# Optimization experiments

Measured on AMD Instinct MI355X. Metric: run time of the kernel, lower is better.

Reference implementation:

```python
import jax, jax.numpy as jnp
import numpy as np

N_HASHES = 4
CHUNK = 144
REDUCTION = 4

# PyTorch bicubic (a=-0.75), align_corners=False, integer scale 2 ->
# fixed fractional offsets t=0.75 (even outputs) and t=0.25 (odd outputs).
_EW = jnp.array([-0.03515625, 0.26171875, 0.87890625, -0.10546875], jnp.float32)
_OW = _EW[::-1]


def _up2_axis(x, axis):
    n = x.shape[axis]
    pad = [(0, 0)] * x.ndim
    pad[axis] = (2, 2)
    xp = jnp.pad(x, pad, mode='edge')  # torch clamps border indices
    sl = lambda s: jax.lax.slice_in_dim(xp, s, s + n, axis=axis)
    even = sum(_EW[k] * sl(k) for k in range(4))
    odd = sum(_OW[k] * sl(k + 1) for k in range(4))
    out = jnp.stack([even, odd], axis=axis + 1)
    shp = list(x.shape)
    shp[axis] = 2 * n
    return out.reshape(shp)


def bicubic_up2(x):
    return _up2_axis(_up2_axis(x, 2), 3)


def conv2d(x, w, b, pad):
    y = jax.lax.conv_general_dilated(x, w, (1, 1), [(pad, pad), (pad, pad)],
                                     dimension_numbers=('NCHW', 'OIHW', 'NCHW'))
    return y + b[None, :, None, None]


def _adj(t):
    # attend to own + two adjacent buckets along chunk axis (axis=2)
    return jnp.concatenate([t, jnp.roll(t, 1, axis=2), jnp.roll(t, -1, axis=2)], axis=3)


def nlsa(x, wm, bm, wa, ba, rot):
    N, Cc, H, W = x.shape
    L = H * W
    xe = conv2d(x, wm, bm, 1).reshape(N, -1, L).transpose(0, 2, 1)  # [N,L,C]
    ye = conv2d(x, wa, ba, 0).reshape(N, -1, L).transpose(0, 2, 1)  # [N,L,C*red]
    C = xe.shape[-1]
    hash_buckets = min(L // CHUNK + (L // CHUNK) % 2, 128)
    # LSH: random rotations -> argmax bucket codes (non-differentiable, detached)
    rotated = jnp.einsum('btf,fhi->bhti', xe, rot)  # [N,h,L,hb//2]
    rotated = jnp.concatenate([rotated, -rotated], axis=-1)  # [N,h,L,hb]
    codes = jnp.argmax(rotated, axis=-1)  # [N,h,L]
    codes = codes + (jnp.arange(N_HASHES) * hash_buckets)[None, :, None]
    codes = jax.lax.stop_gradient(codes.reshape(N, -1))  # [N,h*L]
    indices = jnp.argsort(codes, axis=-1)
    undo = jnp.argsort(indices, axis=-1)
    mod = indices % L
    xs = jnp.take_along_axis(xe, mod[..., None], axis=1)  # [N,h*L,C]
    ys = jnp.take_along_axis(ye, mod[..., None], axis=1)  # [N,h*L,C*red]
    padding = (-L) % CHUNK
    xb = xs.reshape(N, N_HASHES, L, C)
    yb = ys.reshape(N, N_HASHES, L, C * REDUCTION)
    if padding:
        xb = jnp.concatenate([xb, xb[:, :, -padding:, :]], axis=2)
        yb = jnp.concatenate([yb, yb[:, :, -padding:, :]], axis=2)
    nch = xb.shape[2] // CHUNK
    xb = xb.reshape(N, N_HASHES, nch, CHUNK, C)
    yb = yb.reshape(N, N_HASHES, nch, CHUNK, C * REDUCTION)
    xm = xb / jnp.maximum(jnp.linalg.norm(xb, axis=-1, keepdims=True), 5e-5)
    xm = _adj(xm)      # [N,h,k,3*chunk,C]
    ybj = _adj(yb)     # [N,h,k,3*chunk,C*red]
    raw = jnp.einsum('bhkie,bhkje->bhkij', xb, xm)  # [N,h,k,chunk,3*chunk]
    bscore = jax.scipy.special.logsumexp(raw, axis=-1, keepdims=True)
    score = jnp.exp(raw - bscore)
    ret = jnp.einsum('bhkij,bhkje->bhkie', score, ybj)
    ret = ret.reshape(N, N_HASHES, -1, C * REDUCTION)
    bscore = bscore.reshape(N, N_HASHES, -1)
    if padding:
        ret = ret[:, :, :-padding]
        bscore = bscore[:, :, :-padding]
    ret = ret.reshape(N, -1, C * REDUCTION)
    bscore = bscore.reshape(N, -1)
    ret = jnp.take_along_axis(ret, undo[..., None], axis=1)
    bscore = jnp.take_along_axis(bscore, undo, axis=1)
    ret = ret.reshape(N, N_HASHES, L, C * REDUCTION)
    probs = jax.nn.softmax(bscore.reshape(N, N_HASHES, L, 1), axis=1)
    ret = jnp.sum(ret * probs, axis=1)  # [N,L,C*red]
    return ret.transpose(0, 2, 1).reshape(N, -1, H, W) + x


def setup_inputs() -> dict:
    key = jax.random.key(0)
    ks = jax.random.split(key, 8)
    w = lambda k, shape, fan: (jax.random.normal(k, shape, jnp.float32) / np.sqrt(fan)).astype(jnp.float32)
    return {
        'x': jax.random.normal(ks[0], (2, 64, 96, 96), jnp.float32),
        'w1': w(ks[1], (64, 64, 3, 3), 64 * 9), 'b1': jnp.zeros((64,), jnp.float32),
        'w2': w(ks[2], (64, 64, 3, 3), 64 * 9), 'b2': jnp.zeros((64,), jnp.float32),
        'wm': w(ks[3], (16, 64, 3, 3), 64 * 9), 'bm': jnp.zeros((16,), jnp.float32),
        'wa': w(ks[4], (64, 64, 1, 1), 64), 'ba': jnp.zeros((64,), jnp.float32),
        'rot': jax.random.normal(ks[5], (16, N_HASHES, 64), jnp.float32),  # [C, h, hash_buckets//2]
    }


def reference(x, w1, b1, w2, b2, wm, bm, wa, ba, rot):
    x = bicubic_up2(x)
    x = jax.nn.relu(conv2d(x, w1, b1, 1))
    x = jax.nn.relu(conv2d(x, w2, b2, 1))
    return nlsa(x, wm, bm, wa, ba, rot)
```

## Files before the change

kernel.cpp:

```cpp
#include <hip/hip_runtime.h>
#include <math.h>

#define NB 2
#define CIN 64
#define H0 96
#define W0 96
#define HH 192
#define WW 192
#define LL (HH*WW)
#define NHASH 4
#define CHK 144
#define NCHK 256
#define CE 16
#define NBUCK 128
#define SEGL 576
#define NSEG 64
#define PW 194
#define PS ((size_t)NB*PW*PW*64)

#define K_ROWB   80
#define V_ROWB   912
#define P_ROWB   72
#define VT_SZB   58368
#define PST_SZB  10368
#define LKI_SZB  1728
#define LDS_T1   (VT_SZB + PST_SZB + LKI_SZB)
#define CONV_LDS (2*4*66*64*2)

typedef __attribute__((ext_vector_type(8))) short short8_t;
typedef __attribute__((ext_vector_type(4))) float f32x4;
union FragU { unsigned int u[4]; int4 i; short8_t s; };

__device__ __forceinline__ unsigned int cvtpk_bf16(float a, float b){
  unsigned int r;
  asm("v_cvt_pk_bf16_f32 %0, %1, %2" : "=v"(r) : "v"(a), "v"(b));
  return r;
}
__device__ __forceinline__ float bfl(unsigned int u){ return __uint_as_float(u << 16); }
__device__ __forceinline__ float bfh(unsigned int u){ return __uint_as_float(u & 0xffff0000u); }

__global__ __launch_bounds__(256) void k_zerob(unsigned short* pA, unsigned short* pB){
  const int cid = blockIdx.x*256 + threadIdx.x;
  if (cid >= 4*2*772*8) return;
  const int chunk = cid & 7;
  int cell = cid >> 3;
  const int plane = cell / (2*772); cell -= plane*(2*772);
  const int n = cell / 772; int b = cell - n*772;
  int ypad, xpad;
  if (b < 194){ ypad = 0; xpad = b; }
  else if (b < 388){ ypad = 193; xpad = b-194; }
  else if (b < 580){ ypad = b-388+1; xpad = 0; }
  else { ypad = b-580+1; xpad = 193; }
  unsigned short* base = (plane < 2 ? pA : pB) + (size_t)(plane & 1)*PS;
  *(uint4*)(base + (((size_t)n*PW + ypad)*PW + xpad)*64 + chunk*8) =
      make_uint4(0u,0u,0u,0u);
}

__global__ __launch_bounds__(256) void k_upsample2(const float* __restrict__ x,
    unsigned short* __restrict__ oh, unsigned short* __restrict__ ol){
  __shared__ unsigned int pk[64][65];
  const int t = threadIdx.x;
  const int bx = blockIdx.x, oy = blockIdx.y, n = blockIdx.z;
  const int oxl = t & 63, cq = t >> 6;
  const int ox = bx*64 + oxl;
  const int i = oy >> 1, a = oy & 1;
  const int j = ox >> 1, b = ox & 1;
  const float e0=-0.03515625f, e1=0.26171875f, e2=0.87890625f, e3=-0.10546875f;
  float wy[4], wx[4]; int ty[4], tx[4];
  if (a){ wy[0]=e3; wy[1]=e2; wy[2]=e1; wy[3]=e0; } else { wy[0]=e0; wy[1]=e1; wy[2]=e2; wy[3]=e3; }
  if (b){ wx[0]=e3; wx[1]=e2; wx[2]=e1; wx[3]=e0; } else { wx[0]=e0; wx[1]=e1; wx[2]=e2; wx[3]=e3; }
  const int offy = a ? -1 : -2, offx = b ? -1 : -2;
  #pragma unroll
  for (int k=0;k<4;k++){
    int u = i + offy + k; ty[k] = u<0?0:(u>H0-1?H0-1:u);
    int s = j + offx + k; tx[k] = s<0?0:(s>W0-1?W0-1:s);
  }
  for (int ci = cq*16; ci < cq*16+16; ++ci){
    const float* xp = x + ((size_t)n*CIN + ci)*(H0*W0);
    float s = 0.f;
    #pragma unroll
    for (int ky=0;ky<4;ky++){
      const float* row = xp + ty[ky]*W0;
      float rs = 0.f;
      rs = fmaf(wx[0], row[tx[0]], rs);
      rs = fmaf(wx[1], row[tx[1]], rs);
      rs = fmaf(wx[2], row[tx[2]], rs);
      rs = fmaf(wx[3], row[tx[3]], rs);
      s = fmaf(wy[ky], rs, s);
    }
    unsigned int hu = cvtpk_bf16(s, s);
    unsigned int lu = cvtpk_bf16(s - bfl(hu), 0.f);
    pk[oxl][ci] = (hu & 0xffffu) | (lu << 16);
  }
  __syncthreads();
  const size_t rowb = (((size_t)n*PW + oy+1)*PW + bx*64 + 1)*64;
  for (int e = t; e < 1024; e += 256){
    const int plane = e >> 9, r2 = e & 511;
    const int ox2 = r2 >> 3, c8 = r2 & 7;
    const int xpad = bx*64 + ox2 + 1;
    const int grp = (c8 ^ (xpad & 7))*8;
    unsigned int a0=pk[ox2][grp+0], a1=pk[ox2][grp+1], a2=pk[ox2][grp+2], a3=pk[ox2][grp+3];
    unsigned int a4=pk[ox2][grp+4], a5=pk[ox2][grp+5], a6=pk[ox2][grp+6], a7=pk[ox2][grp+7];
    uint4 wv;
    if (plane == 0){
      wv.x = (a0&0xffffu)|(a1<<16); wv.y = (a2&0xffffu)|(a3<<16);
      wv.z = (a4&0xffffu)|(a5<<16); wv.w = (a6&0xffffu)|(a7<<16);
    } else {
      wv.x = (a0>>16)|(a1&0xffff0000u); wv.y = (a2>>16)|(a3&0xffff0000u);
      wv.z = (a4>>16)|(a5&0xffff0000u); wv.w = (a6>>16)|(a7&0xffff0000u);
    }
    *(uint4*)((plane ? ol : oh) + rowb + (size_t)ox2*64 + c8*8) = wv;
  }
}

__global__ __launch_bounds__(256) void k_prepw(const float* __restrict__ w,
    unsigned short* __restrict__ wsT, int CO){
  int idx = blockIdx.x*256 + threadIdx.x;
  if (idx >= CO*64*9) return;
  int tap = idx % 9; int rem = idx / 9;
  int ci = rem % 64; int co = rem / 64;
  float v = w[(size_t)(co*64 + ci)*9 + tap];
  unsigned int hu = cvtpk_bf16(v, v) & 0xffffu;
  float hf = bfl(hu);
  unsigned int lu = cvtpk_bf16(v - hf, 0.f) & 0xffffu;
  int half = ci >> 5, kg = (ci >> 3) & 3, e = ci & 7;
  size_t base = ((size_t)(tap*2 + half)*2)*CO*32 + ((size_t)co*4 + kg)*8 + e;
  wsT[base]         = (unsigned short)hu;
  wsT[base + (size_t)CO*32] = (unsigned short)lu;
}

template<int CO, int OMODE>
__global__ __launch_bounds__(256) void k_conv3s(const unsigned short* __restrict__ inh,
    const unsigned short* __restrict__ inl, const unsigned short* __restrict__ wsT,
    const float* __restrict__ bias, unsigned short* __restrict__ outh,
    unsigned short* __restrict__ outl, float* __restrict__ outf){
  extern __shared__ char cvsm[];
  unsigned short (*inH)[66][64] = (unsigned short (*)[66][64])cvsm;
  unsigned short (*inL)[66][64] = (unsigned short (*)[66][64])(cvsm + 33792);
  const int t = threadIdx.x;
  const int bx = blockIdx.x, by = blockIdx.y, n = blockIdx.z;
  const int y0 = by*2, x0 = bx*64;
  const int l = t & 63, w = t >> 6;
  const int lq = l & 15, kg = l >> 4;

  const size_t gbase = (((size_t)n*PW + y0)*PW + x0)*64;
  for (int e = t; e < 4224; e += 256){
    const int plane = (e >= 2112);
    const int rem = e - plane*2112;
    const int row = rem / 528;
    const int cw = rem - row*528;
    const unsigned short* src = (plane ? inl : inh) + gbase + (size_t)row*(PW*64) + cw*8;
    *(uint4*)(cvsm + plane*33792 + row*8448 + cw*16) = *(const uint4*)src;
  }
  __syncthreads();

  constexpr int NCT = CO/16;
  f32x4 acc0[NCT], acc1[NCT];
  #pragma unroll
  for (int c=0;c<NCT;c++){ acc0[c] = (f32x4){0.f,0.f,0.f,0.f}; acc1[c] = acc0[c]; }
  const unsigned short* wlane = wsT + (size_t)lq*32 + (size_t)kg*8;

  #pragma unroll
  for (int tap=0; tap<9; ++tap){
    const int ky = tap/3, kx = tap - ky*3;
    const int col = w*16 + lq + kx;
    #pragma unroll
    for (int half=0; half<2; ++half){
      const int sci = ((((half<<2) | kg) ^ (col & 7)) << 3);
      FragU Bh0, Bl0, Bh1, Bl1;
      Bh0.i = *(const int4*)&inH[ky  ][col][sci];
      Bl0.i = *(const int4*)&inL[ky  ][col][sci];
      Bh1.i = *(const int4*)&inH[ky+1][col][sci];
      Bl1.i = *(const int4*)&inL[ky+1][col][sci];
      const unsigned short* wth = wlane + (size_t)((tap*2+half)*2)*CO*32;
      #pragma unroll
      for (int ct=0; ct<NCT; ++ct){
        FragU Ah, Al;
        Ah.i = *(const int4*)(wth + ct*512);
        Al.i = *(const int4*)(wth + CO*32 + ct*512);
        acc0[ct] = __builtin_amdgcn_mfma_f32_16x16x32_bf16(Ah.s, Bl0.s, acc0[ct], 0,0,0);
        acc0[ct] = __builtin_amdgcn_mfma_f32_16x16x32_bf16(Al.s, Bh0.s, acc0[ct], 0,0,0);
        acc0[ct] = __builtin_amdgcn_mfma_f32_16x16x32_bf16(Ah.s, Bh0.s, acc0[ct], 0,0,0);
        acc1[ct] = __builtin_amdgcn_mfma_f32_16x16x32_bf16(Ah.s, Bl1.s, acc1[ct], 0,0,0);
        acc1[ct] = __builtin_amdgcn_mfma_f32_16x16x32_bf16(Al.s, Bh1.s, acc1[ct], 0,0,0);
        acc1[ct] = __builtin_amdgcn_mfma_f32_16x16x32_bf16(Ah.s, Bh1.s, acc1[ct], 0,0,0);
      }
    }
  }

  const int px = x0 + w*16 + lq;
  const int xpad = px + 1;
  const int xg = xpad & 7;
  if constexpr (OMODE == 2){
    #pragma unroll
    for (int r=0; r<4; ++r){
      const int co = kg*4 + r;
      const float bv = bias[co];
      outf[((size_t)n*LL + (size_t)(y0  )*WW + px)*16 + co] = acc0[0][r] + bv;
      outf[((size_t)n*LL + (size_t)(y0+1)*WW + px)*16 + co] = acc1[0][r] + bv;
    }
  } else {
    #pragma unroll
    for (int ct=0; ct<NCT; ++ct){
      const int ci = ct*16 + kg*4;
      const int sgrp = (ct*2 + (kg>>1)) ^ xg;
      #pragma unroll
      for (int row=0; row<2; ++row){
        const f32x4& A = row ? acc1[ct] : acc0[ct];
        float v0 = fmaxf(A[0] + bias[ci+0], 0.f);
        float v1 = fmaxf(A[1] + bias[ci+1], 0.f);
        float v2 = fmaxf(A[2] + bias[ci+2], 0.f);
        float v3 = fmaxf(A[3] + bias[ci+3], 0.f);
        const unsigned int h0 = cvtpk_bf16(v0, v1);
        const unsigned int h1 = cvtpk_bf16(v2, v3);
        const unsigned int l0 = cvtpk_bf16(v0 - bfl(h0), v1 - bfh(h0));
        const unsigned int l1 = cvtpk_bf16(v2 - bfl(h1), v3 - bfh(h1));
        const size_t off = (((size_t)n*PW + (y0+row+1))*PW + xpad)*64 + sgrp*8 + (kg&1)*4;
        *(uint2*)(outh + off) = make_uint2(h0, h1);
        *(uint2*)(outl + off) = make_uint2(l0, l1);
        if constexpr (OMODE == 1){
          *(float4*)&outf[(((size_t)n*LL + (size_t)(y0+row)*WW + px)*64) + ci] =
              make_float4(v0, v1, v2, v3);
        }
      }
    }
  }
}

__global__ __launch_bounds__(256) void k_conv1x1(const float* __restrict__ x2,
    const float* __restrict__ wa, const float* __restrict__ ba,
    unsigned short* __restrict__ yeB){
  __shared__ float xs[64][65];
  __shared__ float wts[64][65];
  const int t = threadIdx.x;
  const int n = blockIdx.y;
  const int l0 = blockIdx.x*64;
  for (int e=t; e<4096; e+=256){
    int lv = e >> 6, ci = e & 63;
    xs[ci][lv]  = x2[((size_t)n*LL + l0 + lv)*64 + ci];
    wts[ci][lv] = wa[(size_t)lv*64 + ci];
  }
  __syncthreads();
  const int l = t & 63, cq = t >> 6;
  float acc[16];
  #pragma unroll
  for (int i=0;i<16;i++) acc[i] = ba[cq*16+i];
  for (int ci=0; ci<64; ci++){
    float xv = xs[ci][l];
    #pragma unroll
    for (int i=0;i<16;i++) acc[i] = fmaf(xv, wts[ci][cq*16+i], acc[i]);
  }
  unsigned int wds[8];
  #pragma unroll
  for (int i=0;i<8;i++) wds[i] = cvtpk_bf16(acc[2*i], acc[2*i+1]);
  uint4* op = (uint4*)&yeB[((size_t)n*LL + l0 + l)*64 + cq*16];
  op[0] = make_uint4(wds[0],wds[1],wds[2],wds[3]);
  op[1] = make_uint4(wds[4],wds[5],wds[6],wds[7]);
}

__global__ __launch_bounds__(128) void k_codes(const float* __restrict__ xe,
    const float* __restrict__ rot, unsigned char* __restrict__ codes){
  __shared__ float rs[NHASH][64][16];
  const int t = threadIdx.x;
  for (int e=t; e<4096; e+=128){
    int f = e >> 8; int rem = e & 255;
    int h = rem >> 6; int i = rem & 63;
    rs[h][i][f] = rot[((size_t)f*NHASH + h)*64 + i];
  }
  __syncthreads();
  const int n = blockIdx.y;
  const int l = blockIdx.x*128 + t;
  float q[16];
  const float* xr = &xe[((size_t)n*LL + l)*16];
  #pragma unroll
  for (int f=0;f<16;f++) q[f] = xr[f];
  #pragma unroll
  for (int h=0;h<NHASH;h++){
    float bp = -3.0e38f, bn = -3.0e38f; int ap=0, an=0;
    for (int i=0;i<64;i++){
      float s = 0.f;
      #pragma unroll
      for (int f=0;f<16;f++) s = fmaf(q[f], rs[h][i][f], s);
      if (s > bp){ bp = s; ap = i; }
      if (-s > bn){ bn = -s; an = i; }
    }
    int code = (bp >= bn) ? ap : (64 + an);
    codes[((size_t)n*NHASH + h)*LL + l] = (unsigned char)code;
  }
}

__global__ __launch_bounds__(256) void k_hist(const unsigned char* __restrict__ codes,
    unsigned int* __restrict__ segHist){
  __shared__ unsigned int h[NBUCK];
  const int t = threadIdx.x;
  if (t < NBUCK) h[t] = 0;
  __syncthreads();
  const int n = blockIdx.z, hh = blockIdx.y, s = blockIdx.x;
  const unsigned char* cp = codes + ((size_t)n*NHASH + hh)*LL + (size_t)s*SEGL;
  for (int e=t; e<SEGL; e+=256) atomicAdd(&h[cp[e]], 1u);
  __syncthreads();
  if (t < NBUCK)
    segHist[(((size_t)(n*NHASH+hh))*NSEG + s)*NBUCK + t] = h[t];
}

__global__ __launch_bounds__(128) void k_scan(unsigned int* __restrict__ segHist){
  __shared__ unsigned int tot[NBUCK];
  __shared__ unsigned int base[NBUCK];
  const int b = threadIdx.x;
  const size_t off = (size_t)blockIdx.x * NSEG * NBUCK;
  unsigned int run = 0;
  for (int s=0;s<NSEG;s++){
    unsigned int v = segHist[off + (size_t)s*NBUCK + b];
    segHist[off + (size_t)s*NBUCK + b] = run;
    run += v;
  }
  tot[b] = run;
  __syncthreads();
  if (b==0){ unsigned int r=0; for (int i=0;i<NBUCK;i++){ base[i]=r; r+=tot[i]; } }
  __syncthreads();
  const unsigned int bb = base[b];
  for (int s=0;s<NSEG;s++) segHist[off + (size_t)s*NBUCK + b] += bb;
}

__global__ __launch_bounds__(256) void k_rank(const unsigned char* __restrict__ codes,
    const unsigned int* __restrict__ segHist, int* __restrict__ sortPos,
    int* __restrict__ srtIdx){
  __shared__ unsigned int cw[SEGL/4];
  __shared__ unsigned int sbase[NBUCK];
  const int t = threadIdx.x;
  const int n = blockIdx.z, hh = blockIdx.y, s = blockIdx.x;
  const size_t cb = ((size_t)n*NHASH + hh)*LL + (size_t)s*SEGL;
  const unsigned int* cp32 = (const unsigned int*)(codes + cb);
  for (int e=t; e<SEGL/4; e+=256) cw[e] = cp32[e];
  if (t < NBUCK)
    sbase[t] = segHist[(((size_t)(n*NHASH+hh))*NSEG + s)*NBUCK + t];
  __syncthreads();
  const size_t ob = ((size_t)n*NHASH + hh)*LL;
  for (int e=t; e<SEGL; e+=256){
    unsigned int c = (cw[e>>2] >> ((e&3)*8)) & 0xffu;
    unsigned int mul = c * 0x01010101u;
    int cnt = 0;
    const int nw = e >> 2;
    for (int wi=0; wi<nw; wi++){
      unsigned int v = cw[wi] ^ mul;
      unsigned int t1 = (v & 0x7f7f7f7fu) + 0x7f7f7f7fu;
      unsigned int z = ~(t1 | v) & 0x80808080u;
      cnt += __popc(z);
    }
    unsigned int lastw = cw[nw];
    const int nbp = e & 3;
    for (int bp=0; bp<nbp; bp++)
      if (((lastw >> (bp*8)) & 0xffu) == c) cnt++;
    int pos = (int)sbase[c] + cnt;
    int lx = s*SEGL + e;
    sortPos[ob + lx] = pos;
    srtIdx[ob + pos] = lx;
  }
}

__global__ __launch_bounds__(256) void k_gatherK(const float* __restrict__ xe,
    const int* __restrict__ srtIdx, unsigned short* __restrict__ Ksrt,
    float* __restrict__ normQ){
  const int idx = blockIdx.x*256 + threadIdx.x;
  if (idx >= NB*NHASH*LL) return;
  const int n = idx / (NHASH*LL);
  const int lk = srtIdx[idx];
  const float4* xr = (const float4*)&xe[((size_t)n*LL + lk)*16];
  float4 v0 = xr[0], v1 = xr[1], v2 = xr[2], v3 = xr[3];
  float f[16] = {v0.x,v0.y,v0.z,v0.w, v1.x,v1.y,v1.z,v1.w,
                 v2.x,v2.y,v2.z,v2.w, v3.x,v3.y,v3.z,v3.w};
  float ss = 0.f;
  #pragma unroll
  for (int i=0;i<16;i++) ss = fmaf(f[i], f[i], ss);
  const float nq = sqrtf(ss);
  normQ[idx] = nq;
  const float inv = 1.f / fmaxf(nq, 5e-5f);
  #pragma unroll
  for (int i=0;i<16;i++) f[i] *= inv;
  unsigned int kh[8], klo[8];
  #pragma unroll
  for (int i=0;i<8;i++) kh[i] = cvtpk_bf16(f[2*i], f[2*i+1]);
  #pragma unroll
  for (int i=0;i<8;i++)
    klo[i] = cvtpk_bf16(f[2*i] - bfl(kh[i]), f[2*i+1] - bfh(kh[i]));
  int4* kr = (int4*)(Ksrt + (size_t)idx*32);
  kr[0] = make_int4((int)kh[0],(int)kh[1],(int)kh[2],(int)kh[3]);
  kr[1] = make_int4((int)kh[4],(int)kh[5],(int)kh[6],(int)kh[7]);
  kr[2] = make_int4((int)klo[0],(int)klo[1],(int)klo[2],(int)klo[3]);
  kr[3] = make_int4((int)klo[4],(int)klo[5],(int)klo[6],(int)klo[7]);
}

__global__ __launch_bounds__(576) void k_attn2(const unsigned short* __restrict__ yeB,
    const int* __restrict__ srtIdx, const unsigned short* __restrict__ Ksrt,
    const float* __restrict__ normQ, unsigned short* __restrict__ retS,
    float* __restrict__ bscore){
  extern __shared__ char smem[];
  char* Vt  = smem;
  char* Pst = Vt + VT_SZB;
  int* lkI  = (int*)(Pst + PST_SZB);

  const int t = threadIdx.x;
  const int k = blockIdx.x, hh = blockIdx.y, n = blockIdx.z;
  const size_t sb = ((size_t)n*NHASH + hh)*LL;
  const int l = t & 63, w = t >> 6;
  const int lq16 = l & 15, g = l >> 4;

  if (t < 432){
    const int c3 = t / CHK, jl = t - c3*CHK;
    const int kc = (c3==0) ? k : ((c3==1) ? ((k+NCHK-1)&(NCHK-1)) : ((k+1)&(NCHK-1)));
    lkI[t] = srtIdx[sb + (size_t)kc*CHK + jl];
  }
  if (t < 512){
    int c = t >> 3, jp = t & 7;
    *(unsigned int*)(Vt + c*V_ROWB + 864 + jp*4) = 0u;
  }
  __syncthreads();

  #pragma unroll 4
  for (int it=0; it<24; ++it){
    const int e = t + it*576;
    const int jp = e >> 6, c = e & 63;
    const unsigned int a = yeB[((size_t)n*LL + lkI[2*jp  ])*64 + c];
    const unsigned int b = yeB[((size_t)n*LL + lkI[2*jp+1])*64 + c];
    *(unsigned int*)(Vt + c*V_ROWB + jp*4) = a | (b << 16);
  }
  const int qg = w*16 + lq16;
  const int pq = k*CHK + qg;
  FragU b1, b2;
  const unsigned short* qrow = Ksrt + (sb + pq)*32;
  b1.i = *(const int4*)(qrow + (g&1)*8);
  if (g < 2) b2.i = *(const int4*)(qrow + 16 + (g&1)*8);
  else { b2.u[0]=0u; b2.u[1]=0u; b2.u[2]=0u; b2.u[3]=0u; }
  const float nq_ = normQ[sb + pq];
  const float msc = fmaxf(nq_, 5e-5f);
  __syncthreads();

  float sum = 0.f;
  f32x4 O0 = {0.f,0.f,0.f,0.f}, O1 = O0, O2 = O0, O3 = O0;
  char* Pw = Pst + w*(16*P_ROWB);
  for (int u=0; u<14; ++u){
    #pragma unroll
    for (int sub=0; sub<2; ++sub){
      const int t27 = u*2 + sub;
      uint2 pw;
      if (t27 < 27){
        const int c3 = t27 / 9;
        const int kc = (c3==0) ? k : ((c3==1) ? ((k+NCHK-1)&(NCHK-1)) : ((k+1)&(NCHK-1)));
        const int row16 = (t27 - c3*9)*16;
        FragU a; a.i = *(const int4*)(Ksrt + (sb + (size_t)kc*CHK + row16 + lq16)*32 + g*8);
        f32x4 C = {0.f,0.f,0.f,0.f};
        C = __builtin_amdgcn_mfma_f32_16x16x32_bf16(a.s, b2.s, C, 0, 0, 0);
        C = __builtin_amdgcn_mfma_f32_16x16x32_bf16(a.s, b1.s, C, 0, 0, 0);
        const float p0 = __expf(fmaf(msc, C[0], -nq_));
        const float p1 = __expf(fmaf(msc, C[1], -nq_));
        const float p2 = __expf(fmaf(msc, C[2], -nq_));
        const float p3 = __expf(fmaf(msc, C[3], -nq_));
        sum += (p0+p1) + (p2+p3);
        pw = make_uint2(cvtpk_bf16(p0,p1), cvtpk_bf16(p2,p3));
      } else {
        pw = make_uint2(0u, 0u);
      }
      *(uint2*)(Pw + lq16*P_ROWB + sub*32 + g*8) = pw;
    }
    asm volatile("s_waitcnt lgkmcnt(0)" ::: "memory");
    __builtin_amdgcn_sched_barrier(0);
    FragU bp; bp.i = *(const int4*)(Pw + lq16*P_ROWB + g*16);
    const char* Vb = Vt + lq16*V_ROWB + u*64 + g*16;
    FragU av;
    av.i = *(const int4*)(Vb);             O0 = __builtin_amdgcn_mfma_f32_16x16x32_bf16(av.s, bp.s, O0, 0,0,0);
    av.i = *(const int4*)(Vb + 16*V_ROWB); O1 = __builtin_amdgcn_mfma_f32_16x16x32_bf16(av.s, bp.s, O1, 0,0,0);
    av.i = *(const int4*)(Vb + 32*V_ROWB); O2 = __builtin_amdgcn_mfma_f32_16x16x32_bf16(av.s, bp.s, O2, 0,0,0);
    av.i = *(const int4*)(Vb + 48*V_ROWB); O3 = __builtin_amdgcn_mfma_f32_16x16x32_bf16(av.s, bp.s, O3, 0,0,0);
  }
  sum += __shfl_xor(sum, 16);
  sum += __shfl_xor(sum, 32);
  const float linv = 1.f / sum;

  unsigned short* op = &retS[(sb + pq)*64];
  {
    uint2 s0 = make_uint2(cvtpk_bf16(O0[0]*linv, O0[1]*linv), cvtpk_bf16(O0[2]*linv, O0[3]*linv));
    uint2 s1 = make_uint2(cvtpk_bf16(O1[0]*linv, O1[1]*linv), cvtpk_bf16(O1[2]*linv, O1[3]*linv));
    uint2 s2 = make_uint2(cvtpk_bf16(O2[0]*linv, O2[1]*linv), cvtpk_bf16(O2[2]*linv, O2[3]*linv));
    uint2 s3 = make_uint2(cvtpk_bf16(O3[0]*linv, O3[1]*linv), cvtpk_bf16(O3[2]*linv, O3[3]*linv));
    *(uint2*)(op +  0 + g*4) = s0;
    *(uint2*)(op + 16 + g*4) = s1;
    *(uint2*)(op + 32 + g*4) = s2;
    *(uint2*)(op + 48 + g*4) = s3;
  }
  if (g == 0) bscore[sb + pq] = nq_ + logf(sum);
}

__global__ __launch_bounds__(256) void k_combine(const unsigned short* __restrict__ retS,
    const float* __restrict__ bscore, const int* __restrict__ sortPos,
    const float* __restrict__ x2, float* __restrict__ out){
  const int idx = blockIdx.x*256 + threadIdx.x;
  if (idx >= NB*LL) return;
  const int l = idx % LL, n = idx / LL;
  float bs[NHASH]; int pp[NHASH];
  #pragma unroll
  for (int h=0;h<NHASH;h++){
    size_t sb = ((size_t)n*NHASH + h)*LL;
    int p = sortPos[sb + l];
    pp[h] = p; bs[h] = bscore[sb + p];
  }
  float m = fmaxf(fmaxf(bs[0],bs[1]), fmaxf(bs[2],bs[3]));
  float wsum = 0.f; float wv[NHASH];
  #pragma unroll
  for (int h=0;h<NHASH;h++){ wv[h] = expf(bs[h]-m); wsum += wv[h]; }
  const float winv = 1.f / wsum;
  float o[64];
  #pragma unroll
  for (int i=0;i<64;i++) o[i]=0.f;
  #pragma unroll
  for (int h=0;h<NHASH;h++){
    const float wh = wv[h]*winv;
    const uint4* rp = (const uint4*)&retS[(((size_t)n*NHASH + h)*LL + pp[h])*64];
    #pragma unroll
    for (int i2=0;i2<8;i2++){
      uint4 v = rp[i2];
      o[i2*8+0] = fmaf(wh, bfl(v.x), o[i2*8+0]);
      o[i2*8+1] = fmaf(wh, bfh(v.x), o[i2*8+1]);
      o[i2*8+2] = fmaf(wh, bfl(v.y), o[i2*8+2]);
      o[i2*8+3] = fmaf(wh, bfh(v.y), o[i2*8+3]);
      o[i2*8+4] = fmaf(wh, bfl(v.z), o[i2*8+4]);
      o[i2*8+5] = fmaf(wh, bfh(v.z), o[i2*8+5]);
      o[i2*8+6] = fmaf(wh, bfl(v.w), o[i2*8+6]);
      o[i2*8+7] = fmaf(wh, bfh(v.w), o[i2*8+7]);
    }
  }
  const float4* xr = (const float4*)&x2[((size_t)n*LL + l)*64];
  #pragma unroll
  for (int c4=0; c4<16; ++c4){
    float4 xv = xr[c4];
    out[((size_t)n*64 + c4*4+0)*LL + l] = o[c4*4+0] + xv.x;
    out[((size_t)n*64 + c4*4+1)*LL + l] = o[c4*4+1] + xv.y;
    out[((size_t)n*64 + c4*4+2)*LL + l] = o[c4*4+2] + xv.z;
    out[((size_t)n*64 + c4*4+3)*LL + l] = o[c4*4+3] + xv.w;
  }
}

extern "C" void kernel_launch(void* const* d_in, const int* in_sizes, int n_in,
                              void* d_out, int out_size, void* d_ws, size_t ws_size,
                              hipStream_t stream){
  const float* x   = (const float*)d_in[0];
  const float* w1  = (const float*)d_in[1];
  const float* b1  = (const float*)d_in[2];
  const float* w2  = (const float*)d_in[3];
  const float* b2  = (const float*)d_in[4];
  const float* wm  = (const float*)d_in[5];
  const float* bm  = (const float*)d_in[6];
  const float* wa  = (const float*)d_in[7];
  const float* ba  = (const float*)d_in[8];
  const float* rot = (const float*)d_in[9];
  float* outp = (float*)d_out;
  char* ws = (char*)d_ws;
  const size_t FM   = (size_t)NB*CIN*HH*WW*sizeof(float);
  const size_t YEB  = (size_t)NB*LL*64*2;
  const size_t RETB = (size_t)NB*NHASH*LL*64*2;
  const size_t NHL4 = (size_t)NB*NHASH*LL*4;

  char* p = ws;
  unsigned short* yeB = (unsigned short*)p;  p += YEB;
  char* regA = p;                            p += RETB;
  float* x2  = (float*)p;                    p += FM;
  float* xe  = (float*)p;                    p += (size_t)NB*LL*CE*sizeof(float);
  unsigned char* codes = (unsigned char*)p;  p += (size_t)NB*NHASH*LL;
  unsigned int* segHist = (unsigned int*)p;  p += (size_t)NB*NHASH*NSEG*NBUCK*4;
  int* sortPos = (int*)p;                    p += NHL4;
  int* srtIdx  = (int*)p;                    p += NHL4;
  float* bscore = (float*)p;                 p += NHL4;
  unsigned short* wsT1 = (unsigned short*)p; p += (size_t)9*2*2*64*32*2;
  unsigned short* wsT2 = (unsigned short*)p; p += (size_t)9*2*2*64*32*2;
  unsigned short* wsTm = (unsigned short*)p; p += (size_t)9*2*2*16*32*2;
  unsigned short* Ksrt = (unsigned short*)p; p += (size_t)NB*NHASH*LL*32*2;
  float* normQ = (float*)p;                  p += NHL4;
  const size_t needT1 = (size_t)(p - ws);
  if (ws_size < needT1) return;

  unsigned short* retS = (unsigned short*)regA;
  unsigned short* pairA = (unsigned short*)regA;
  unsigned short* pairB = Ksrt;

  hipFuncSetAttribute((const void*)k_attn2,
                      hipFuncAttributeMaxDynamicSharedMemorySize, LDS_T1);
  hipFuncSetAttribute((const void*)k_conv3s<64,0>,
                      hipFuncAttributeMaxDynamicSharedMemorySize, CONV_LDS);
  hipFuncSetAttribute((const void*)k_conv3s<64,1>,
                      hipFuncAttributeMaxDynamicSharedMemorySize, CONV_LDS);
  hipFuncSetAttribute((const void*)k_conv3s<16,2>,
                      hipFuncAttributeMaxDynamicSharedMemorySize, CONV_LDS);

  k_prepw<<<dim3((64*64*9+255)/256), dim3(256), 0, stream>>>(w1, wsT1, 64);
  k_prepw<<<dim3((64*64*9+255)/256), dim3(256), 0, stream>>>(w2, wsT2, 64);
  k_prepw<<<dim3((16*64*9+255)/256), dim3(256), 0, stream>>>(wm, wsTm, 16);
  k_zerob<<<dim3((4*2*772*8+255)/256), dim3(256), 0, stream>>>(pairA, pairB);
  k_upsample2<<<dim3(WW/64, HH, NB), dim3(256), 0, stream>>>(x, pairA, pairA + PS);
  k_conv3s<64,0><<<dim3(3, HH/2, NB), dim3(256), CONV_LDS, stream>>>(
      pairA, pairA + PS, wsT1, b1, pairB, pairB + PS, nullptr);
  k_conv3s<64,1><<<dim3(3, HH/2, NB), dim3(256), CONV_LDS, stream>>>(
      pairB, pairB + PS, wsT2, b2, pairA, pairA + PS, x2);
  k_conv3s<16,2><<<dim3(3, HH/2, NB), dim3(256), CONV_LDS, stream>>>(
      pairA, pairA + PS, wsTm, bm, nullptr, nullptr, xe);
  k_conv1x1<<<dim3(LL/64, NB), dim3(256), 0, stream>>>(x2, wa, ba, yeB);
  k_codes<<<dim3(LL/128, NB), dim3(128), 0, stream>>>(xe, rot, codes);
  k_hist<<<dim3(NSEG, NHASH, NB), dim3(256), 0, stream>>>(codes, segHist);
  k_scan<<<dim3(NB*NHASH), dim3(128), 0, stream>>>(segHist);
  k_rank<<<dim3(NSEG, NHASH, NB), dim3(256), 0, stream>>>(codes, segHist, sortPos, srtIdx);
  k_gatherK<<<dim3((NB*NHASH*LL+255)/256), dim3(256), 0, stream>>>(xe, srtIdx, Ksrt, normQ);
  k_attn2<<<dim3(NCHK, NHASH, NB), dim3(576), LDS_T1, stream>>>(
      yeB, srtIdx, Ksrt, normQ, retS, bscore);
  k_combine<<<dim3((NB*LL+255)/256), dim3(256), 0, stream>>>(retS, bscore, sortPos, x2, outp);
}
```

Measured before the change: 349.3 us.

## Double-buffer V tiles in attention kernel to shrink LDS and overlap gathers

The attention kernel no longer gathers the full 432-key V block into LDS up front. It streams 32-key V slices into a small double buffer, prefetching the next slice while the current one is used for MFMA. This cuts LDS per block from about 70KB to about 21KB, which may allow more resident blocks per CU. In exchange it adds a block-wide barrier every iteration and issues the global gathers in smaller, latency-exposed batches.

```diff
diff --git a/kernel.cpp b/kernel.cpp
--- a/kernel.cpp
+++ b/kernel.cpp
@@ -18,13 +18,12 @@
 #define PW 194
 #define PS ((size_t)NB*PW*PW*64)
 
-#define K_ROWB   80
-#define V_ROWB   912
 #define P_ROWB   72
-#define VT_SZB   58368
 #define PST_SZB  10368
 #define LKI_SZB  1728
-#define LDS_T1   (VT_SZB + PST_SZB + LKI_SZB)
+#define V6_ROWB  72
+#define V6_BUF   (64*V6_ROWB)
+#define LDS_A6   (PST_SZB + LKI_SZB + 2*V6_BUF)
 #define CONV_LDS (2*4*66*64*2)
 
 typedef __attribute__((ext_vector_type(8))) short short8_t;
@@ -390,14 +389,14 @@
   kr[3] = make_int4((int)klo[4],(int)klo[5],(int)klo[6],(int)klo[7]);
 }
 
-__global__ __launch_bounds__(576) void k_attn2(const unsigned short* __restrict__ yeB,
+__global__ __launch_bounds__(576) void k_attn6(const unsigned short* __restrict__ yeB,
     const int* __restrict__ srtIdx, const unsigned short* __restrict__ Ksrt,
     const float* __restrict__ normQ, unsigned short* __restrict__ retS,
     float* __restrict__ bscore){
   extern __shared__ char smem[];
-  char* Vt  = smem;
-  char* Pst = Vt + VT_SZB;
-  int* lkI  = (int*)(Pst + PST_SZB);
+  char* Pst = smem;
+  int* lkI  = (int*)(smem + PST_SZB);
+  char* Vb  = smem + PST_SZB + LKI_SZB;
 
   const int t = threadIdx.x;
   const int k = blockIdx.x, hh = blockIdx.y, n = blockIdx.z;
@@ -410,19 +409,13 @@
     const int kc = (c3==0) ? k : ((c3==1) ? ((k+NCHK-1)&(NCHK-1)) : ((k+1)&(NCHK-1)));
     lkI[t] = srtIdx[sb + (size_t)kc*CHK + jl];
   }
-  if (t < 512){
-    int c = t >> 3, jp = t & 7;
-    *(unsigned int*)(Vt + c*V_ROWB + 864 + jp*4) = 0u;
-  }
-  __syncthreads();
-
-  #pragma unroll 4
-  for (int it=0; it<24; ++it){
-    const int e = t + it*576;
-    const int jp = e >> 6, c = e & 63;
-    const unsigned int a = yeB[((size_t)n*LL + lkI[2*jp  ])*64 + c];
-    const unsigned int b = yeB[((size_t)n*LL + lkI[2*jp+1])*64 + c];
-    *(unsigned int*)(Vt + c*V_ROWB + jp*4) = a | (b << 16);
+  __syncthreads();
+
+  for (int e=t; e<1024; e+=576){
+    const int jp = e>>6, c = e&63;
+    const unsigned a = yeB[((size_t)n*LL + lkI[jp*2  ])*64 + c];
+    const unsigned b = yeB[((size_t)n*LL + lkI[jp*2+1])*64 + c];
+    *(unsigned*)(Vb + c*V6_ROWB + jp*4) = a | (b << 16);
   }
   const int qg = w*16 + lq16;
   const int pq = k*CHK + qg;
@@ -438,7 +431,20 @@
   float sum = 0.f;
   f32x4 O0 = {0.f,0.f,0.f,0.f}, O1 = O0, O2 = O0, O3 = O0;
   char* Pw = Pst + w*(16*P_ROWB);
+
   for (int u=0; u<14; ++u){
+    char* const Vcur = Vb + (u&1)*V6_BUF;
+    char* const Vnxt = Vb + ((u+1)&1)*V6_BUF;
+    if (u < 13){
+      const int jb = 32*(u+1);
+      for (int e=t; e<1024; e+=576){
+        const int jp = e>>6, c = e&63;
+        const int j0 = jb + jp*2;
+        const unsigned a = (j0   < 432) ? (unsigned)yeB[((size_t)n*LL + lkI[j0  ])*64 + c] : 0u;
+        const unsigned b = (j0+1 < 432) ? (unsigned)yeB[((size_t)n*LL + lkI[j0+1])*64 + c] : 0u;
+        *(unsigned*)(Vnxt + c*V6_ROWB + jp*4) = a | (b << 16);
+      }
+    }
     #pragma unroll
     for (int sub=0; sub<2; ++sub){
       const int t27 = u*2 + sub;
@@ -465,12 +471,13 @@
     asm volatile("s_waitcnt lgkmcnt(0)" ::: "memory");
     __builtin_amdgcn_sched_barrier(0);
     FragU bp; bp.i = *(const int4*)(Pw + lq16*P_ROWB + g*16);
-    const char* Vb = Vt + lq16*V_ROWB + u*64 + g*16;
+    const char* Vr = Vcur + lq16*V6_ROWB + g*16;
     FragU av;
-    av.i = *(const int4*)(Vb);             O0 = __builtin_amdgcn_mfma_f32_16x16x32_bf16(av.s, bp.s, O0, 0,0,0);
-    av.i = *(const int4*)(Vb + 16*V_ROWB); O1 = __builtin_amdgcn_mfma_f32_16x16x32_bf16(av.s, bp.s, O1, 0,0,0);
-    av.i = *(const int4*)(Vb + 32*V_ROWB); O2 = __builtin_amdgcn_mfma_f32_16x16x32_bf16(av.s, bp.s, O2, 0,0,0);
-    av.i = *(const int4*)(Vb + 48*V_ROWB); O3 = __builtin_amdgcn_mfma_f32_16x16x32_bf16(av.s, bp.s, O3, 0,0,0);
+    av.i = *(const int4*)(Vr);              O0 = __builtin_amdgcn_mfma_f32_16x16x32_bf16(av.s, bp.s, O0, 0,0,0);
+    av.i = *(const int4*)(Vr + 16*V6_ROWB); O1 = __builtin_amdgcn_mfma_f32_16x16x32_bf16(av.s, bp.s, O1, 0,0,0);
+    av.i = *(const int4*)(Vr + 32*V6_ROWB); O2 = __builtin_amdgcn_mfma_f32_16x16x32_bf16(av.s, bp.s, O2, 0,0,0);
+    av.i = *(const int4*)(Vr + 48*V6_ROWB); O3 = __builtin_amdgcn_mfma_f32_16x16x32_bf16(av.s, bp.s, O3, 0,0,0);
+    __syncthreads();
   }
   sum += __shfl_xor(sum, 16);
   sum += __shfl_xor(sum, 32);
@@ -581,8 +588,8 @@
   unsigned short* pairA = (unsigned short*)regA;
   unsigned short* pairB = Ksrt;
 
-  hipFuncSetAttribute((const void*)k_attn2,
-                      hipFuncAttributeMaxDynamicSharedMemorySize, LDS_T1);
+  hipFuncSetAttribute((const void*)k_attn6,
+                      hipFuncAttributeMaxDynamicSharedMemorySize, LDS_A6);
   hipFuncSetAttribute((const void*)k_conv3s<64,0>,
                       hipFuncAttributeMaxDynamicSharedMemorySize, CONV_LDS);
   hipFuncSetAttribute((const void*)k_conv3s<64,1>,
@@ -607,7 +614,7 @@
   k_scan<<<dim3(NB*NHASH), dim3(128), 0, stream>>>(segHist);
   k_rank<<<dim3(NSEG, NHASH, NB), dim3(256), 0, stream>>>(codes, segHist, sortPos, srtIdx);
   k_gatherK<<<dim3((NB*NHASH*LL+255)/256), dim3(256), 0, stream>>>(xe, srtIdx, Ksrt, normQ);
-  k_attn2<<<dim3(NCHK, NHASH, NB), dim3(576), LDS_T1, stream>>>(
+  k_attn6<<<dim3(NCHK, NHASH, NB), dim3(576), LDS_A6, stream>>>(
       yeB, srtIdx, Ksrt, normQ, retS, bscore);
   k_combine<<<dim3((NB*LL+255)/256), dim3(256), 0, stream>>>(retS, bscore, sortPos, x2, outp);
 }
```

Measured after the change: 491.2 us. +40.6%, slower.
